# Kernel tuning notes

Hardware: AMD Instinct MI355X
Metric: run time of the kernel (lower is better)

Reference implementation:

```python
import jax, jax.numpy as jnp
import numpy as np

B, S, H = 1, 2048, 1024
E, K, F = 8, 2, 4096
LN_EPS = 1e-5
GATE_EPS = 1e-8
STD = 0.02


def setup_inputs() -> dict:
    key = jax.random.key(0)
    ks = jax.random.split(key, 5)
    return {
        "x": jax.random.normal(ks[0], (B, S, H), jnp.float32),
        "ln_w": jnp.ones((H,), jnp.float32),
        "ln_b": jnp.zeros((H,), jnp.float32),
        "gate_w": jax.random.normal(ks[1], (E, H), jnp.float32) * STD,
        "Wg": jax.random.normal(ks[2], (E, F, H), jnp.float32) * STD,
        "Wu": jax.random.normal(ks[3], (E, F, H), jnp.float32) * STD,
        "Wd": jax.random.normal(ks[4], (E, H, F), jnp.float32) * STD,
    }


def _layernorm(x, w, b):
    mu = x.mean(-1, keepdims=True)
    var = x.var(-1, keepdims=True)
    return (x - mu) * jax.lax.rsqrt(var + LN_EPS) * w + b


def reference(x, ln_w, ln_b, gate_w, Wg, Wu, Wd):
    normed = _layernorm(x, ln_w, ln_b)           # (B,S,H)
    xf = normed.reshape(-1, H)                   # (T,H), T=B*S

    # --- gating (temperature = 1.0) ---
    logits = xf @ gate_w.T                       # (T,E)
    probs = jax.nn.softmax(logits, axis=-1)
    gates, idx = jax.lax.top_k(probs, K)         # (T,K)
    gates = gates / (gates.sum(-1, keepdims=True) + GATE_EPS)

    oneh = jax.nn.one_hot(idx, E, dtype=xf.dtype)        # (T,K,E)
    combine = (oneh * gates[..., None]).sum(1)           # (T,E) per-expert weight per token

    # load-balance aux loss (torch .var() is unbiased, ddof=1)
    counts = oneh.sum((0, 1))                            # (E,)
    usage = counts / counts.sum()
    lbl = (jnp.var(usage, ddof=1) / (usage.mean() + GATE_EPS)) ** 2

    # --- experts: SwiGLU variant (gate * silu(up)) across all experts ---
    g = jnp.einsum('th,efh->etf', xf, Wg)                # (E,T,F)
    u = jnp.einsum('th,efh->etf', xf, Wu)
    y = jnp.einsum('etf,ehf->eth', g * jax.nn.silu(u), Wd)  # (E,T,H)

    moe = jnp.einsum('te,eth->th', combine, y)           # (T,H)
    out = x + moe.reshape(B, S, H)                       # residual
    return out, lbl
```

## Files before the change

kernel.cpp:

```cpp
#include <hip/hip_runtime.h>
#include <hip/hip_bf16.h>

#define T_ 2048
#define H_ 1024
#define E_ 8
#define F_ 4096

#define BM 128
#define BN 128
#define BK 32

typedef __attribute__((ext_vector_type(8))) short short8;
typedef __attribute__((ext_vector_type(4))) float f32x4;

__device__ __forceinline__ unsigned short f2bf(float f) {
    union { float f; unsigned u; } a; a.f = f;
    unsigned r = a.u + 0x7fffu + ((a.u >> 16) & 1u);
    return (unsigned short)(r >> 16);
}

__device__ __forceinline__ short8 pack8(float4 a, float4 b) {
    short8 r;
    r[0] = (short)f2bf(a.x); r[1] = (short)f2bf(a.y);
    r[2] = (short)f2bf(a.z); r[3] = (short)f2bf(a.w);
    r[4] = (short)f2bf(b.x); r[5] = (short)f2bf(b.y);
    r[6] = (short)f2bf(b.z); r[7] = (short)f2bf(b.w);
    return r;
}

__device__ __forceinline__ void gld_lds16(const void* g, void* l) {
    __builtin_amdgcn_global_load_lds(
        (const __attribute__((address_space(1))) unsigned int*)g,
        (__attribute__((address_space(3))) unsigned int*)l,
        16, 0, 0);
}

__global__ __launch_bounds__(256) void convert_kernel(
    const float* __restrict__ src, unsigned short* __restrict__ dst, int n8)
{
    int i = blockIdx.x * blockDim.x + threadIdx.x;
    int stride = gridDim.x * blockDim.x;
    for (; i < n8; i += stride) {
        const float4* s = reinterpret_cast<const float4*>(src + (size_t)i * 8);
        float4 a = s[0], b = s[1];
        reinterpret_cast<short8*>(dst)[i] = pack8(a, b);
    }
}

__global__ __launch_bounds__(256) void ln_gate_kernel(
    const float* __restrict__ x, const float* __restrict__ lnw,
    const float* __restrict__ lnb, const float* __restrict__ gatew,
    float* __restrict__ out, unsigned short* __restrict__ xn,
    int* __restrict__ tok, float* __restrict__ gwslot, int* __restrict__ cnt)
{
    int t = blockIdx.x;
    int tid = threadIdx.x;
    const float4* xr = reinterpret_cast<const float4*>(x + (size_t)t * H_);
    float4 v = xr[tid];
    float s  = v.x + v.y + v.z + v.w;
    float ss = v.x*v.x + v.y*v.y + v.z*v.z + v.w*v.w;
    #pragma unroll
    for (int off = 32; off >= 1; off >>= 1) {
        s  += __shfl_xor(s, off);
        ss += __shfl_xor(ss, off);
    }
    __shared__ float redS[4], redQ[4];
    __shared__ float gred[4][E_];
    int wv = tid >> 6;
    if ((tid & 63) == 0) { redS[wv] = s; redQ[wv] = ss; }
    __syncthreads();
    s  = redS[0] + redS[1] + redS[2] + redS[3];
    ss = redQ[0] + redQ[1] + redQ[2] + redQ[3];
    float mu  = s * (1.0f / H_);
    float var = ss * (1.0f / H_) - mu * mu;
    float inv = rsqrtf(var + 1e-5f);

    float4 w4 = reinterpret_cast<const float4*>(lnw)[tid];
    float4 b4 = reinterpret_cast<const float4*>(lnb)[tid];
    float n0 = (v.x - mu) * inv * w4.x + b4.x;
    float n1 = (v.y - mu) * inv * w4.y + b4.y;
    float n2 = (v.z - mu) * inv * w4.z + b4.z;
    float n3 = (v.w - mu) * inv * w4.w + b4.w;

    ushort4 pk = make_ushort4(f2bf(n0), f2bf(n1), f2bf(n2), f2bf(n3));
    reinterpret_cast<ushort4*>(xn + (size_t)t * H_)[tid] = pk;
    reinterpret_cast<float4*>(out + (size_t)t * H_)[tid] = v;

    float lg[E_];
    #pragma unroll
    for (int e = 0; e < E_; ++e) {
        float4 g4 = reinterpret_cast<const float4*>(gatew + (size_t)e * H_)[tid];
        lg[e] = n0*g4.x + n1*g4.y + n2*g4.z + n3*g4.w;
    }
    #pragma unroll
    for (int e = 0; e < E_; ++e) {
        #pragma unroll
        for (int off = 32; off >= 1; off >>= 1)
            lg[e] += __shfl_xor(lg[e], off);
    }
    if ((tid & 63) == 0) {
        #pragma unroll
        for (int e = 0; e < E_; ++e) gred[wv][e] = lg[e];
    }
    __syncthreads();
    if (tid == 0) {
        float logit[E_]; float mx = -1e30f;
        #pragma unroll
        for (int e = 0; e < E_; ++e) {
            logit[e] = gred[0][e] + gred[1][e] + gred[2][e] + gred[3][e];
            mx = fmaxf(mx, logit[e]);
        }
        float p[E_]; float sum = 0.f;
        #pragma unroll
        for (int e = 0; e < E_; ++e) { p[e] = expf(logit[e] - mx); sum += p[e]; }
        int i0 = 0;
        #pragma unroll
        for (int e = 1; e < E_; ++e) if (logit[e] > logit[i0]) i0 = e;
        int i1 = (i0 == 0) ? 1 : 0;
        #pragma unroll
        for (int e = 0; e < E_; ++e) if (e != i0 && logit[e] > logit[i1]) i1 = e;
        float p0 = p[i0] / sum, p1 = p[i1] / sum;
        float dn = p0 + p1 + 1e-8f;
        float w0 = p0 / dn, w1 = p1 / dn;
        int pos0 = atomicAdd(&cnt[i0], 1);
        tok[i0 * T_ + pos0] = t; gwslot[i0 * T_ + pos0] = w0;
        int pos1 = atomicAdd(&cnt[i1], 1);
        tok[i1 * T_ + pos1] = t; gwslot[i1 * T_ + pos1] = w1;
    }
}

__global__ void finalize_kernel(const int* __restrict__ cnt, int* __restrict__ offs,
                                float* __restrict__ lbl_out)
{
    if (threadIdx.x == 0 && blockIdx.x == 0) {
        int c[E_]; int tot = 0;
        #pragma unroll
        for (int e = 0; e < E_; ++e) { c[e] = cnt[e]; tot += c[e]; }
        int o = 0;
        #pragma unroll
        for (int e = 0; e < E_; ++e) { offs[e] = o; o += c[e]; }
        float itot = 1.0f / (float)tot;
        float u[E_]; float mean = 0.f;
        #pragma unroll
        for (int e = 0; e < E_; ++e) { u[e] = c[e] * itot; mean += u[e]; }
        mean *= (1.0f / E_);
        float var = 0.f;
        #pragma unroll
        for (int e = 0; e < E_; ++e) { float d = u[e] - mean; var += d * d; }
        var *= (1.0f / (E_ - 1));
        float l = var / (mean + 1e-8f);
        lbl_out[0] = l * l;
    }
}


__global__ __launch_bounds__(256) void gu_fast(
    const unsigned short* __restrict__ Wgb, const unsigned short* __restrict__ Wub,
    const unsigned short* __restrict__ xn,
    const int* __restrict__ tok, const int* __restrict__ cnt,
    const int* __restrict__ offs, unsigned short* __restrict__ hbuf)
{
    int fj = blockIdx.x, ti = blockIdx.y, e = blockIdx.z;
    int Te = cnt[e];
    int base = ti * BM;
    if (base >= Te) return;
    int rows = Te - base; if (rows > BM) rows = BM;

    __shared__ unsigned short As[BM * BK];
    __shared__ unsigned short Bg[BN * BK];
    __shared__ unsigned short Bu[BN * BK];
    __shared__ int toks[BM];

    int tid = threadIdx.x;
    if (tid < BM) {
        int r = base + tid;
        toks[tid] = tok[e * T_ + (r < Te ? r : Te - 1)];
    }
    __syncthreads();

    int w = tid >> 6, l = tid & 63;
    int lr = l & 15, kc = l >> 4;
    int r0   = w * 16 + (l >> 2);
    int csrc = (l & 3) ^ ((l >> 3) & 3);

    const unsigned short* agA = xn + (size_t)toks[r0]      * H_ + csrc * 8;
    const unsigned short* agB = xn + (size_t)toks[r0 + 64] * H_ + csrc * 8;
    const unsigned short* bg0 = Wgb + ((size_t)e * F_ + (size_t)fj * BN + r0) * H_ + csrc * 8;
    const unsigned short* bg1 = bg0 + (size_t)64 * H_;
    const unsigned short* bu0 = Wub + ((size_t)e * F_ + (size_t)fj * BN + r0) * H_ + csrc * 8;
    const unsigned short* bu1 = bu0 + (size_t)64 * H_;

    char* AsB = (char*)As; char* BgB = (char*)Bg; char* BuB = (char*)Bu;

    f32x4 zero4 = {0.f, 0.f, 0.f, 0.f};
    f32x4 accg[4][4], accu[4][4];
    #pragma unroll
    for (int m = 0; m < 4; ++m)
        #pragma unroll
        for (int n = 0; n < 4; ++n) { accg[m][n] = zero4; accu[m][n] = zero4; }

    int wr = w >> 1, wc = w & 1;

    for (int it = 0; it < H_ / BK; ++it) {
        int k0 = it * BK;
        __syncthreads();
        gld_lds16(agA + k0, AsB + w * 1024);
        gld_lds16(agB + k0, AsB + 4096 + w * 1024);
        gld_lds16(bg0 + k0, BgB + w * 1024);
        gld_lds16(bg1 + k0, BgB + 4096 + w * 1024);
        gld_lds16(bu0 + k0, BuB + w * 1024);
        gld_lds16(bu1 + k0, BuB + 4096 + w * 1024);
        __syncthreads();

        short8 af[4];
        #pragma unroll
        for (int m = 0; m < 4; ++m) {
            int rowA = wr * 64 + m * 16 + lr;
            int sA = kc ^ ((rowA >> 1) & 3);
            af[m] = *(const short8*)(AsB + rowA * 64 + sA * 16);
        }
        #pragma unroll
        for (int n = 0; n < 4; ++n) {
            int rowB = wc * 64 + n * 16 + lr;
            int sB = kc ^ ((rowB >> 1) & 3);
            short8 bgn = *(const short8*)(BgB + rowB * 64 + sB * 16);
            #pragma unroll
            for (int m = 0; m < 4; ++m)
                accg[m][n] = __builtin_amdgcn_mfma_f32_16x16x32_bf16(af[m], bgn, accg[m][n], 0, 0, 0);
        }
        #pragma unroll
        for (int n = 0; n < 4; ++n) {
            int rowB = wc * 64 + n * 16 + lr;
            int sB = kc ^ ((rowB >> 1) & 3);
            short8 bun = *(const short8*)(BuB + rowB * 64 + sB * 16);
            #pragma unroll
            for (int m = 0; m < 4; ++m)
                accu[m][n] = __builtin_amdgcn_mfma_f32_16x16x32_bf16(af[m], bun, accu[m][n], 0, 0, 0);
        }
    }

    size_t slotbase = (size_t)offs[e] + base;
    #pragma unroll
    for (int m = 0; m < 4; ++m) {
        #pragma unroll
        for (int n = 0; n < 4; ++n) {
            int col = fj * BN + wc * 64 + n * 16 + lr;
            #pragma unroll
            for (int q = 0; q < 4; ++q) {
                int row = wr * 64 + m * 16 + (l >> 4) * 4 + q;
                if (row < rows) {
                    float uu = accu[m][n][q];
                    float hh = accg[m][n][q] * (uu / (1.f + expf(-uu)));
                    hbuf[(slotbase + row) * F_ + col] = f2bf(hh);
                }
            }
        }
    }
}

__global__ __launch_bounds__(256) void down_fast(
    const unsigned short* __restrict__ Wdb, const unsigned short* __restrict__ hbuf,
    const int* __restrict__ tok, const int* __restrict__ cnt,
    const int* __restrict__ offs, const float* __restrict__ gwslot,
    float* __restrict__ out)
{
    int hj = blockIdx.x, ti = blockIdx.y, e = blockIdx.z;
    int Te = cnt[e];
    int base = ti * BM;
    if (base >= Te) return;
    int rows = Te - base; if (rows > BM) rows = BM;

    __shared__ unsigned short As[BM * BK];
    __shared__ unsigned short Bs[BN * BK];

    int tid = threadIdx.x;
    int w = tid >> 6, l = tid & 63;
    int lr = l & 15, kc = l >> 4;
    int r0   = w * 16 + (l >> 2);
    int csrc = (l & 3) ^ ((l >> 3) & 3);

    size_t slot0 = (size_t)offs[e] + base;
    size_t arA = slot0 + r0;      if (arA > (size_t)(T_ * 2 - 1)) arA = T_ * 2 - 1;
    size_t arB = slot0 + r0 + 64; if (arB > (size_t)(T_ * 2 - 1)) arB = T_ * 2 - 1;
    const unsigned short* agA = hbuf + arA * F_ + csrc * 8;
    const unsigned short* agB = hbuf + arB * F_ + csrc * 8;
    const unsigned short* bd0 = Wdb + ((size_t)e * H_ + (size_t)hj * BN + r0) * F_ + csrc * 8;
    const unsigned short* bd1 = bd0 + (size_t)64 * F_;

    char* AsB = (char*)As; char* BsB = (char*)Bs;

    f32x4 zero4 = {0.f, 0.f, 0.f, 0.f};
    f32x4 acc[4][4];
    #pragma unroll
    for (int m = 0; m < 4; ++m)
        #pragma unroll
        for (int n = 0; n < 4; ++n) acc[m][n] = zero4;

    int wr = w >> 1, wc = w & 1;

    for (int it = 0; it < F_ / BK; ++it) {
        int k0 = it * BK;
        __syncthreads();
        gld_lds16(agA + k0, AsB + w * 1024);
        gld_lds16(agB + k0, AsB + 4096 + w * 1024);
        gld_lds16(bd0 + k0, BsB + w * 1024);
        gld_lds16(bd1 + k0, BsB + 4096 + w * 1024);
        __syncthreads();

        short8 af[4];
        #pragma unroll
        for (int m = 0; m < 4; ++m) {
            int rowA = wr * 64 + m * 16 + lr;
            int sA = kc ^ ((rowA >> 1) & 3);
            af[m] = *(const short8*)(AsB + rowA * 64 + sA * 16);
        }
        #pragma unroll
        for (int n = 0; n < 4; ++n) {
            int rowB = wc * 64 + n * 16 + lr;
            int sB = kc ^ ((rowB >> 1) & 3);
            short8 bn = *(const short8*)(BsB + rowB * 64 + sB * 16);
            #pragma unroll
            for (int m = 0; m < 4; ++m)
                acc[m][n] = __builtin_amdgcn_mfma_f32_16x16x32_bf16(af[m], bn, acc[m][n], 0, 0, 0);
        }
    }

    #pragma unroll
    for (int m = 0; m < 4; ++m) {
        #pragma unroll
        for (int q = 0; q < 4; ++q) {
            int row = wr * 64 + m * 16 + (l >> 4) * 4 + q;
            if (row < rows) {
                int   tkn = tok[e * T_ + base + row];
                float wt  = gwslot[e * T_ + base + row];
                #pragma unroll
                for (int n = 0; n < 4; ++n) {
                    int col = hj * BN + wc * 64 + n * 16 + lr;
                    atomicAdd(&out[(size_t)tkn * H_ + col], wt * acc[m][n][q]);
                }
            }
        }
    }
}

__global__ __launch_bounds__(256) void gu_kernel(
    const float* __restrict__ Wg, const float* __restrict__ Wu,
    const unsigned short* __restrict__ xn,
    const int* __restrict__ tok, const int* __restrict__ cnt,
    const int* __restrict__ offs, unsigned short* __restrict__ hbuf)
{
    int ti = blockIdx.x, fj = blockIdx.y, e = blockIdx.z;
    int Te = cnt[e];
    int base = ti * BM;
    if (base >= Te) return;
    int rows = Te - base; if (rows > BM) rows = BM;

    __shared__ unsigned short As[BM][BK];
    __shared__ unsigned short Bgs[BN][BK];
    __shared__ unsigned short Bus[BN][BK];
    __shared__ int toks[BM];

    int tid = threadIdx.x;
    if (tid < BM) {
        int r = base + tid;
        toks[tid] = tok[e * T_ + (r < Te ? r : Te - 1)];
    }
    __syncthreads();

    int w = tid >> 6, l = tid & 63;
    int lr = l & 15, kb8 = (l >> 4) * 8;
    int arow0 = tid >> 2, achk = tid & 3;
    const unsigned short* ag0 = xn + (size_t)toks[arow0]      * H_ + achk * 8;
    const unsigned short* ag1 = xn + (size_t)toks[arow0 + 64] * H_ + achk * 8;

    int brow = tid >> 1, bhalf = tid & 1;
    const float* wgp = Wg + ((size_t)e * F_ + (size_t)fj * BN + brow) * H_ + bhalf * 16;
    const float* wup = Wu + ((size_t)e * F_ + (size_t)fj * BN + brow) * H_ + bhalf * 16;

    f32x4 zero4 = {0.f, 0.f, 0.f, 0.f};
    f32x4 accg[4][4], accu[4][4];
    #pragma unroll
    for (int m = 0; m < 4; ++m)
        #pragma unroll
        for (int n = 0; n < 4; ++n) { accg[m][n] = zero4; accu[m][n] = zero4; }

    for (int it = 0; it < H_ / BK; ++it) {
        int k0 = it * BK;
        __syncthreads();
        gld_lds16(ag0 + k0, (char*)&As[0][0] + w * 1024);
        gld_lds16(ag1 + k0, (char*)&As[0][0] + 4096 + w * 1024);
        float4 g0 = *(const float4*)(wgp + k0);
        float4 g1 = *(const float4*)(wgp + k0 + 4);
        float4 g2 = *(const float4*)(wgp + k0 + 8);
        float4 g3 = *(const float4*)(wgp + k0 + 12);
        float4 u0 = *(const float4*)(wup + k0);
        float4 u1 = *(const float4*)(wup + k0 + 4);
        float4 u2 = *(const float4*)(wup + k0 + 8);
        float4 u3 = *(const float4*)(wup + k0 + 12);
        *(short8*)(&Bgs[brow][bhalf * 16])     = pack8(g0, g1);
        *(short8*)(&Bgs[brow][bhalf * 16 + 8]) = pack8(g2, g3);
        *(short8*)(&Bus[brow][bhalf * 16])     = pack8(u0, u1);
        *(short8*)(&Bus[brow][bhalf * 16 + 8]) = pack8(u2, u3);
        __syncthreads();

        int wr = w >> 1, wc = w & 1;
        short8 af[4];
        #pragma unroll
        for (int m = 0; m < 4; ++m)
            af[m] = *(const short8*)&As[wr * 64 + m * 16 + lr][kb8];
        #pragma unroll
        for (int n = 0; n < 4; ++n) {
            short8 bgn = *(const short8*)&Bgs[wc * 64 + n * 16 + lr][kb8];
            #pragma unroll
            for (int m = 0; m < 4; ++m)
                accg[m][n] = __builtin_amdgcn_mfma_f32_16x16x32_bf16(af[m], bgn, accg[m][n], 0, 0, 0);
        }
        #pragma unroll
        for (int n = 0; n < 4; ++n) {
            short8 bun = *(const short8*)&Bus[wc * 64 + n * 16 + lr][kb8];
            #pragma unroll
            for (int m = 0; m < 4; ++m)
                accu[m][n] = __builtin_amdgcn_mfma_f32_16x16x32_bf16(af[m], bun, accu[m][n], 0, 0, 0);
        }
    }

    int wr = w >> 1, wc = w & 1;
    size_t slotbase = (size_t)offs[e] + base;
    #pragma unroll
    for (int m = 0; m < 4; ++m) {
        #pragma unroll
        for (int n = 0; n < 4; ++n) {
            int col = fj * BN + wc * 64 + n * 16 + lr;
            #pragma unroll
            for (int q = 0; q < 4; ++q) {
                int row = wr * 64 + m * 16 + (l >> 4) * 4 + q;
                if (row < rows) {
                    float uu = accu[m][n][q];
                    float hh = accg[m][n][q] * (uu / (1.f + expf(-uu)));
                    hbuf[(slotbase + row) * F_ + col] = f2bf(hh);
                }
            }
        }
    }
}

__global__ __launch_bounds__(256) void down_kernel(
    const float* __restrict__ Wd, const unsigned short* __restrict__ hbuf,
    const int* __restrict__ tok, const int* __restrict__ cnt,
    const int* __restrict__ offs, const float* __restrict__ gwslot,
    float* __restrict__ out)
{
    int ti = blockIdx.x, hj = blockIdx.y, e = blockIdx.z;
    int Te = cnt[e];
    int base = ti * BM;
    if (base >= Te) return;
    int rows = Te - base; if (rows > BM) rows = BM;

    __shared__ unsigned short As[BM][BK];
    __shared__ unsigned short Bs[BN][BK];

    int tid = threadIdx.x;
    int w = tid >> 6, l = tid & 63;
    int lr = l & 15, kb8 = (l >> 4) * 8;
    int arow0 = tid >> 2, achk = tid & 3;
    size_t slot0 = (size_t)offs[e] + base;
    size_t ar0 = slot0 + arow0;      if (ar0 > (size_t)(T_ * 2 - 1)) ar0 = T_ * 2 - 1;
    size_t ar1 = slot0 + arow0 + 64; if (ar1 > (size_t)(T_ * 2 - 1)) ar1 = T_ * 2 - 1;
    const unsigned short* ag0 = hbuf + ar0 * F_ + achk * 8;
    const unsigned short* ag1 = hbuf + ar1 * F_ + achk * 8;

    int brow = tid >> 1, bhalf = tid & 1;
    const float* wdp = Wd + ((size_t)e * H_ + (size_t)hj * BN + brow) * F_ + bhalf * 16;

    f32x4 zero4 = {0.f, 0.f, 0.f, 0.f};
    f32x4 acc[4][4];
    #pragma unroll
    for (int m = 0; m < 4; ++m)
        #pragma unroll
        for (int n = 0; n < 4; ++n) acc[m][n] = zero4;

    for (int it = 0; it < F_ / BK; ++it) {
        int k0 = it * BK;
        __syncthreads();
        gld_lds16(ag0 + k0, (char*)&As[0][0] + w * 1024);
        gld_lds16(ag1 + k0, (char*)&As[0][0] + 4096 + w * 1024);
        float4 b0 = *(const float4*)(wdp + k0);
        float4 b1 = *(const float4*)(wdp + k0 + 4);
        float4 b2 = *(const float4*)(wdp + k0 + 8);
        float4 b3 = *(const float4*)(wdp + k0 + 12);
        *(short8*)(&Bs[brow][bhalf * 16])     = pack8(b0, b1);
        *(short8*)(&Bs[brow][bhalf * 16 + 8]) = pack8(b2, b3);
        __syncthreads();

        int wr = w >> 1, wc = w & 1;
        short8 af[4];
        #pragma unroll
        for (int m = 0; m < 4; ++m)
            af[m] = *(const short8*)&As[wr * 64 + m * 16 + lr][kb8];
        #pragma unroll
        for (int n = 0; n < 4; ++n) {
            short8 bn = *(const short8*)&Bs[wc * 64 + n * 16 + lr][kb8];
            #pragma unroll
            for (int m = 0; m < 4; ++m)
                acc[m][n] = __builtin_amdgcn_mfma_f32_16x16x32_bf16(af[m], bn, acc[m][n], 0, 0, 0);
        }
    }

    int wr = w >> 1, wc = w & 1;
    #pragma unroll
    for (int m = 0; m < 4; ++m) {
        #pragma unroll
        for (int q = 0; q < 4; ++q) {
            int row = wr * 64 + m * 16 + (l >> 4) * 4 + q;
            if (row < rows) {
                int   tkn = tok[e * T_ + base + row];
                float wt  = gwslot[e * T_ + base + row];
                #pragma unroll
                for (int n = 0; n < 4; ++n) {
                    int col = hj * BN + wc * 64 + n * 16 + lr;
                    atomicAdd(&out[(size_t)tkn * H_ + col], wt * acc[m][n][q]);
                }
            }
        }
    }
}

extern "C" void kernel_launch(void* const* d_in, const int* in_sizes, int n_in,
                              void* d_out, int out_size, void* d_ws, size_t ws_size,
                              hipStream_t stream)
{
    const float* x     = (const float*)d_in[0];
    const float* lnw   = (const float*)d_in[1];
    const float* lnb   = (const float*)d_in[2];
    const float* gatew = (const float*)d_in[3];
    const float* Wg    = (const float*)d_in[4];
    const float* Wu    = (const float*)d_in[5];
    const float* Wd    = (const float*)d_in[6];
    float* out = (float*)d_out;

    char* ws = (char*)d_ws;
    unsigned short* xn     = (unsigned short*)ws;
    int*            tokl   = (int*)  (ws + (4u << 20));
    float*          gwslot = (float*)(ws + (4u << 20) + (64u << 10));
    int*            cnt    = (int*)  (ws + (4u << 20) + (128u << 10));
    int*            offs   = cnt + 16;
    unsigned short* hbuf   = (unsigned short*)(ws + (4u << 20) + (128u << 10) + 256);

    size_t bfw_off = (4u << 20) + (128u << 10) + 256 + (size_t)T_ * 2 * F_ * 2;
    unsigned short* Wgb = (unsigned short*)(ws + bfw_off);
    unsigned short* Wub = Wgb + (size_t)E_ * F_ * H_;
    unsigned short* Wdb = Wub + (size_t)E_ * F_ * H_;
    size_t need_full = bfw_off + 3ull * E_ * F_ * H_ * 2;

    hipMemsetAsync(cnt, 0, 64, stream);
    ln_gate_kernel<<<T_, 256, 0, stream>>>(x, lnw, lnb, gatew, out, xn, tokl, gwslot, cnt);
    finalize_kernel<<<1, 64, 0, stream>>>(cnt, offs, out + (size_t)T_ * H_);

    if (ws_size >= need_full) {
        int n8 = E_ * F_ * H_ / 8;
        convert_kernel<<<8192, 256, 0, stream>>>(Wg, Wgb, n8);
        convert_kernel<<<8192, 256, 0, stream>>>(Wu, Wub, n8);
        convert_kernel<<<8192, 256, 0, stream>>>(Wd, Wdb, n8);
        gu_fast  <<<dim3(F_ / BN, T_ / BM, E_), 256, 0, stream>>>(Wgb, Wub, xn, tokl, cnt, offs, hbuf);
        down_fast<<<dim3(H_ / BN, T_ / BM, E_), 256, 0, stream>>>(Wdb, hbuf, tokl, cnt, offs, gwslot, out);
    } else {
        gu_kernel  <<<dim3(T_ / BM, F_ / BN, E_), 256, 0, stream>>>(Wg, Wu, xn, tokl, cnt, offs, hbuf);
        down_kernel<<<dim3(T_ / BM, H_ / BN, E_), 256, 0, stream>>>(Wd, hbuf, tokl, cnt, offs, gwslot, out);
    }
}
```

Measured before the change: 781.2 us.

## Double-buffer LDS in expert GEMMs, split-K down projection, merge weight conversions

The gate/up and down GEMM kernels now use two LDS buffers per operand and prefetch the next K tile while computing the current one, which cuts one barrier per iteration and hides global-to-LDS load latency. The down projection is split into two K halves across extra grid blocks, doubling the block count for better occupancy; both halves accumulate into the output through the existing atomics. The three weight fp32-to-bf16 conversion launches are merged into one 2D launch. In exchange, LDS use doubles, which may reduce occupancy, and split-K doubles the atomic traffic on the output.

```diff
diff --git a/kernel.cpp b/kernel.cpp
--- a/kernel.cpp
+++ b/kernel.cpp
@@ -35,9 +35,13 @@
         16, 0, 0);
 }
 
-__global__ __launch_bounds__(256) void convert_kernel(
-    const float* __restrict__ src, unsigned short* __restrict__ dst, int n8)
-{
+__global__ __launch_bounds__(256) void convert3_kernel(
+    const float* __restrict__ s0, const float* __restrict__ s1, const float* __restrict__ s2,
+    unsigned short* __restrict__ d0, unsigned short* __restrict__ d1, unsigned short* __restrict__ d2,
+    int n8)
+{
+    const float* src      = blockIdx.y == 0 ? s0 : blockIdx.y == 1 ? s1 : s2;
+    unsigned short* dst   = blockIdx.y == 0 ? d0 : blockIdx.y == 1 ? d1 : d2;
     int i = blockIdx.x * blockDim.x + threadIdx.x;
     int stride = gridDim.x * blockDim.x;
     for (; i < n8; i += stride) {
@@ -166,9 +170,9 @@
     if (base >= Te) return;
     int rows = Te - base; if (rows > BM) rows = BM;
 
-    __shared__ unsigned short As[BM * BK];
-    __shared__ unsigned short Bg[BN * BK];
-    __shared__ unsigned short Bu[BN * BK];
+    __shared__ unsigned short As[2][BM * BK];
+    __shared__ unsigned short Bg[2][BN * BK];
+    __shared__ unsigned short Bu[2][BN * BK];
     __shared__ int toks[BM];
 
     int tid = threadIdx.x;
@@ -190,8 +194,6 @@
     const unsigned short* bu0 = Wub + ((size_t)e * F_ + (size_t)fj * BN + r0) * H_ + csrc * 8;
     const unsigned short* bu1 = bu0 + (size_t)64 * H_;
 
-    char* AsB = (char*)As; char* BgB = (char*)Bg; char* BuB = (char*)Bu;
-
     f32x4 zero4 = {0.f, 0.f, 0.f, 0.f};
     f32x4 accg[4][4], accu[4][4];
     #pragma unroll
@@ -201,16 +203,26 @@
 
     int wr = w >> 1, wc = w & 1;
 
+    {
+        char* A = (char*)As[0]; char* G = (char*)Bg[0]; char* U = (char*)Bu[0];
+        gld_lds16(agA, A + w * 1024); gld_lds16(agB, A + 4096 + w * 1024);
+        gld_lds16(bg0, G + w * 1024); gld_lds16(bg1, G + 4096 + w * 1024);
+        gld_lds16(bu0, U + w * 1024); gld_lds16(bu1, U + 4096 + w * 1024);
+    }
+    __syncthreads();
+
     for (int it = 0; it < H_ / BK; ++it) {
-        int k0 = it * BK;
-        __syncthreads();
-        gld_lds16(agA + k0, AsB + w * 1024);
-        gld_lds16(agB + k0, AsB + 4096 + w * 1024);
-        gld_lds16(bg0 + k0, BgB + w * 1024);
-        gld_lds16(bg1 + k0, BgB + 4096 + w * 1024);
-        gld_lds16(bu0 + k0, BuB + w * 1024);
-        gld_lds16(bu1 + k0, BuB + 4096 + w * 1024);
-        __syncthreads();
+        int cur = it & 1;
+        if (it + 1 < H_ / BK) {
+            int k1 = (it + 1) * BK;
+            char* A = (char*)As[cur ^ 1]; char* G = (char*)Bg[cur ^ 1]; char* U = (char*)Bu[cur ^ 1];
+            gld_lds16(agA + k1, A + w * 1024); gld_lds16(agB + k1, A + 4096 + w * 1024);
+            gld_lds16(bg0 + k1, G + w * 1024); gld_lds16(bg1 + k1, G + 4096 + w * 1024);
+            gld_lds16(bu0 + k1, U + w * 1024); gld_lds16(bu1 + k1, U + 4096 + w * 1024);
+        }
+        const char* AsB = (const char*)As[cur];
+        const char* BgB = (const char*)Bg[cur];
+        const char* BuB = (const char*)Bu[cur];
 
         short8 af[4];
         #pragma unroll
@@ -237,6 +249,7 @@
             for (int m = 0; m < 4; ++m)
                 accu[m][n] = __builtin_amdgcn_mfma_f32_16x16x32_bf16(af[m], bun, accu[m][n], 0, 0, 0);
         }
+        __syncthreads();
     }
 
     size_t slotbase = (size_t)offs[e] + base;
@@ -247,7 +260,7 @@
             int col = fj * BN + wc * 64 + n * 16 + lr;
             #pragma unroll
             for (int q = 0; q < 4; ++q) {
-                int row = wr * 64 + m * 16 + (l >> 4) * 4 + q;
+                int row = wr * 64 + m * 16 + kc * 4 + q;
                 if (row < rows) {
                     float uu = accu[m][n][q];
                     float hh = accg[m][n][q] * (uu / (1.f + expf(-uu)));
@@ -264,30 +277,31 @@
     const int* __restrict__ offs, const float* __restrict__ gwslot,
     float* __restrict__ out)
 {
-    int hj = blockIdx.x, ti = blockIdx.y, e = blockIdx.z;
+    int hj = blockIdx.x, ti = blockIdx.y;
+    int e  = blockIdx.z >> 1, ks = blockIdx.z & 1;
     int Te = cnt[e];
     int base = ti * BM;
     if (base >= Te) return;
     int rows = Te - base; if (rows > BM) rows = BM;
 
-    __shared__ unsigned short As[BM * BK];
-    __shared__ unsigned short Bs[BN * BK];
+    __shared__ unsigned short As[2][BM * BK];
+    __shared__ unsigned short Bs[2][BN * BK];
 
     int tid = threadIdx.x;
     int w = tid >> 6, l = tid & 63;
     int lr = l & 15, kc = l >> 4;
     int r0   = w * 16 + (l >> 2);
     int csrc = (l & 3) ^ ((l >> 3) & 3);
+    const int KOFF = ks * (F_ / 2);
+    const int NT = (F_ / 2) / BK;
 
     size_t slot0 = (size_t)offs[e] + base;
     size_t arA = slot0 + r0;      if (arA > (size_t)(T_ * 2 - 1)) arA = T_ * 2 - 1;
     size_t arB = slot0 + r0 + 64; if (arB > (size_t)(T_ * 2 - 1)) arB = T_ * 2 - 1;
-    const unsigned short* agA = hbuf + arA * F_ + csrc * 8;
-    const unsigned short* agB = hbuf + arB * F_ + csrc * 8;
-    const unsigned short* bd0 = Wdb + ((size_t)e * H_ + (size_t)hj * BN + r0) * F_ + csrc * 8;
+    const unsigned short* agA = hbuf + arA * F_ + KOFF + csrc * 8;
+    const unsigned short* agB = hbuf + arB * F_ + KOFF + csrc * 8;
+    const unsigned short* bd0 = Wdb + ((size_t)e * H_ + (size_t)hj * BN + r0) * F_ + KOFF + csrc * 8;
     const unsigned short* bd1 = bd0 + (size_t)64 * F_;
-
-    char* AsB = (char*)As; char* BsB = (char*)Bs;
 
     f32x4 zero4 = {0.f, 0.f, 0.f, 0.f};
     f32x4 acc[4][4];
@@ -298,14 +312,23 @@
 
     int wr = w >> 1, wc = w & 1;
 
-    for (int it = 0; it < F_ / BK; ++it) {
-        int k0 = it * BK;
-        __syncthreads();
-        gld_lds16(agA + k0, AsB + w * 1024);
-        gld_lds16(agB + k0, AsB + 4096 + w * 1024);
-        gld_lds16(bd0 + k0, BsB + w * 1024);
-        gld_lds16(bd1 + k0, BsB + 4096 + w * 1024);
-        __syncthreads();
+    {
+        char* A = (char*)As[0]; char* B = (char*)Bs[0];
+        gld_lds16(agA, A + w * 1024); gld_lds16(agB, A + 4096 + w * 1024);
+        gld_lds16(bd0, B + w * 1024); gld_lds16(bd1, B + 4096 + w * 1024);
+    }
+    __syncthreads();
+
+    for (int it = 0; it < NT; ++it) {
+        int cur = it & 1;
+        if (it + 1 < NT) {
+            int k1 = (it + 1) * BK;
+            char* A = (char*)As[cur ^ 1]; char* B = (char*)Bs[cur ^ 1];
+            gld_lds16(agA + k1, A + w * 1024); gld_lds16(agB + k1, A + 4096 + w * 1024);
+            gld_lds16(bd0 + k1, B + w * 1024); gld_lds16(bd1 + k1, B + 4096 + w * 1024);
+        }
+        const char* AsB = (const char*)As[cur];
+        const char* BsB = (const char*)Bs[cur];
 
         short8 af[4];
         #pragma unroll
@@ -323,13 +346,14 @@
             for (int m = 0; m < 4; ++m)
                 acc[m][n] = __builtin_amdgcn_mfma_f32_16x16x32_bf16(af[m], bn, acc[m][n], 0, 0, 0);
         }
+        __syncthreads();
     }
 
     #pragma unroll
     for (int m = 0; m < 4; ++m) {
         #pragma unroll
         for (int q = 0; q < 4; ++q) {
-            int row = wr * 64 + m * 16 + (l >> 4) * 4 + q;
+            int row = wr * 64 + m * 16 + kc * 4 + q;
             if (row < rows) {
                 int   tkn = tok[e * T_ + base + row];
                 float wt  = gwslot[e * T_ + base + row];
@@ -558,11 +582,9 @@
 
     if (ws_size >= need_full) {
         int n8 = E_ * F_ * H_ / 8;
-        convert_kernel<<<8192, 256, 0, stream>>>(Wg, Wgb, n8);
-        convert_kernel<<<8192, 256, 0, stream>>>(Wu, Wub, n8);
-        convert_kernel<<<8192, 256, 0, stream>>>(Wd, Wdb, n8);
-        gu_fast  <<<dim3(F_ / BN, T_ / BM, E_), 256, 0, stream>>>(Wgb, Wub, xn, tokl, cnt, offs, hbuf);
-        down_fast<<<dim3(H_ / BN, T_ / BM, E_), 256, 0, stream>>>(Wdb, hbuf, tokl, cnt, offs, gwslot, out);
+        convert3_kernel<<<dim3(2048, 3), 256, 0, stream>>>(Wg, Wu, Wd, Wgb, Wub, Wdb, n8);
+        gu_fast  <<<dim3(F_ / BN, T_ / BM, E_),     256, 0, stream>>>(Wgb, Wub, xn, tokl, cnt, offs, hbuf);
+        down_fast<<<dim3(H_ / BN, T_ / BM, E_ * 2), 256, 0, stream>>>(Wdb, hbuf, tokl, cnt, offs, gwslot, out);
     } else {
         gu_kernel  <<<dim3(T_ / BM, F_ / BN, E_), 256, 0, stream>>>(Wg, Wu, xn, tokl, cnt, offs, hbuf);
         down_kernel<<<dim3(T_ / BM, H_ / BN, E_), 256, 0, stream>>>(Wd, hbuf, tokl, cnt, offs, gwslot, out);
```

Measured after the change: 692.8 us. 1.13x faster.
